# Kernel optimization log

Hardware: AMD Instinct MI355X
Metric: run time of the kernel (lower is better)

The kernel has to match this reference:

```python
import jax, jax.numpy as jnp
import numpy as np

B, S, DE, DR, H, V, R, L = 16, 128, 192, 64, 256, 100000, 64, 12
CAP = 20            # max tree depth enforced at generation time
NLEV = CAP + 1      # number of bottom-up levels (heights 0..CAP)


def setup_inputs() -> dict:
    rng = np.random.default_rng(0)
    # random dependency trees: node 0 is root, parent(i) in [0, i)
    heads = np.full((B, S), -1, np.int64)
    depth = np.zeros((B, S), np.int64)
    for b in range(B):
        for i in range(1, S):
            p = int(rng.integers(0, i))
            if depth[b, p] >= CAP:
                p = 0
            heads[b, i] = p
            depth[b, i] = depth[b, p] + 1
    # height = distance from deepest descendant leaf (leaves: 0)
    height = np.zeros((B, S), np.int64)
    for b in range(B):
        for i in range(S - 1, 0, -1):
            p = heads[b, i]
            if height[b, p] < height[b, i] + 1:
                height[b, p] = height[b, i] + 1
    base = (np.arange(B) * S)[:, None]
    child_idx = (base + np.arange(1, S)[None, :]).reshape(-1)   # [B*(S-1)]
    parent_idx = (base + heads[:, 1:]).reshape(-1)              # [B*(S-1)]

    key = jax.random.key(0)
    ks = jax.random.split(key, 16)
    u = lambda k, shape: jax.random.uniform(k, shape, jnp.float32, -0.08, 0.08)
    DIN = DE + DR
    return {
        "xs": jax.random.randint(ks[0], (B, S), 0, V),
        "rels": jax.random.randint(ks[1], (B, S), 0, R),
        "child_idx": jnp.asarray(child_idx),
        "parent_idx": jnp.asarray(parent_idx),
        "node_height": jnp.asarray(height.reshape(-1)),
        "n_levels": NLEV,
        "emb_W": u(ks[2], (V, DE)),
        "rel_W": u(ks[3], (R, DR)),
        "W_ix": u(ks[4], (DIN, H)), "b_ix": jnp.zeros((H,), jnp.float32),
        "W_ih": u(ks[5], (H, H)),   "b_ih": jnp.zeros((H,), jnp.float32),
        "W_fx": u(ks[6], (DIN, H)), "b_fx": jnp.zeros((H,), jnp.float32),
        "W_fh": u(ks[7], (H, H)),   "b_fh": jnp.zeros((H,), jnp.float32),
        "W_ox": u(ks[8], (DIN, H)), "W_oh": u(ks[9], (H, H)),
        "W_ux": u(ks[10], (DIN, H)), "W_uh": u(ks[11], (H, H)),
        "W_out": u(ks[12], (H, L)), "b_out": jnp.zeros((L,), jnp.float32),
    }


def reference(xs, rels, child_idx, parent_idx, node_height, n_levels,
              emb_W, rel_W, W_ix, b_ix, W_ih, b_ih, W_fx, b_fx, W_fh, b_fh,
              W_ox, W_oh, W_ux, W_uh, W_out, b_out):
    Bs, Ss = xs.shape
    N = Bs * Ss
    Hh = W_ih.shape[0]
    # embed + concat (dropout = identity in eval mode), flatten trees
    x = jnp.concatenate([emb_W[xs], rel_W[rels]], axis=-1).reshape(N, -1)  # [N, DIN]
    # input-side projections are level-invariant: hoist out of the recurrence
    ix = x @ W_ix + b_ix
    fx = x @ W_fx + b_fx
    ox = x @ W_ox
    ux = x @ W_ux

    h0 = jnp.zeros((N, Hh), x.dtype)
    c0 = jnp.zeros((N, Hh), x.dtype)

    def step(carry, level):
        h, c = carry
        h_ch = h[child_idx]                                   # [E, H]
        c_ch = c[child_idx]
        h_sum = jax.ops.segment_sum(h_ch, parent_idx, num_segments=N)
        # per-child forget gate (ChildSum); zero-padded children of the
        # original contribute f*0 = 0, so edges-only is exact
        f_e = jax.nn.sigmoid(h_ch @ W_fh + b_fh + fx[parent_idx])
        fc = jax.ops.segment_sum(f_e * c_ch, parent_idx, num_segments=N)
        i = jax.nn.sigmoid(ix + h_sum @ W_ih + b_ih)
        o = jax.nn.sigmoid(ox + h_sum @ W_oh)
        u_ = jnp.tanh(ux + h_sum @ W_uh)
        c_new = i * u_ + fc
        h_new = o * jnp.tanh(c_new)
        m = (node_height == level)[:, None]                   # commit this level only
        return (jnp.where(m, h_new, h), jnp.where(m, c_new, c)), None

    (h, _), _ = jax.lax.scan(step, (h0, c0), jnp.arange(n_levels))
    pooled = jnp.max(h.reshape(Bs, Ss, Hh), axis=1)           # max_pool1d over time
    return pooled @ W_out + b_out
```

## Files before the change

kernel.cpp:

```cpp
#include <hip/hip_runtime.h>
#include <hip/hip_bf16.h>

#define NN   2048
#define BB   16
#define SS   128
#define HH   256
#define DE   192
#define DR   64
#define DIN  256
#define LOUT 12
#define NLEV 21
#define TE   127

#define NT   16
#define CB   16
#define WC   16
#define RB   16
#define EB   32
#define CPAD 260
#define KP   264

#define SENT64 0xFFFFFFFFFFFFFFFFULL

typedef unsigned long long ull;
typedef __attribute__((ext_vector_type(8))) short short8v;
typedef __attribute__((ext_vector_type(4))) float f32x4;

__device__ __forceinline__ float sigm(float x){ return 1.f/(1.f + __expf(-x)); }

__device__ __forceinline__ short f2bf(float f){
    union { __hip_bfloat16 b; short s; } v; v.b = __float2bfloat16(f); return v.s;
}
__device__ __forceinline__ float bf2f(short s){
    union { unsigned u; float f; } v; v.u = ((unsigned)(unsigned short)s) << 16; return v.f;
}
__device__ __forceinline__ void st_dev(ull* p, ull v){
    __hip_atomic_store(p, v, __ATOMIC_RELAXED, __HIP_MEMORY_SCOPE_AGENT);
}
__device__ __forceinline__ ull ld_dev(const ull* p){
    return __hip_atomic_load(p, __ATOMIC_RELAXED, __HIP_MEMORY_SCOPE_AGENT);
}
__device__ __forceinline__ void st_devf(float* p, float v){
    __hip_atomic_store(p, v, __ATOMIC_RELAXED, __HIP_MEMORY_SCOPE_AGENT);
}
__device__ __forceinline__ int ld_devi(const int* p){
    return __hip_atomic_load(p, __ATOMIC_RELAXED, __HIP_MEMORY_SCOPE_AGENT);
}

__device__ __forceinline__ void barrier_lds(){
    __builtin_amdgcn_sched_barrier(0);
    asm volatile("s_waitcnt lgkmcnt(0)" ::: "memory");
    __builtin_amdgcn_s_barrier();
    __builtin_amdgcn_sched_barrier(0);
}

template<int N>
__device__ __forceinline__ void stageN(const ull* __restrict__ src,
                                       ull* __restrict__ dst){
    ull u[N];
    #pragma unroll
    for (int q = 0; q < N; ++q) u[q] = ld_dev(&src[q]);
    for (;;) {
        bool bad = false;
        #pragma unroll
        for (int q = 0; q < N; ++q) bad = bad || (u[q] == SENT64);
        if (!bad) break;
        __builtin_amdgcn_s_sleep(1);
        #pragma unroll
        for (int q = 0; q < N; ++q)
            if (u[q] == SENT64) u[q] = ld_dev(&src[q]);
    }
    #pragma unroll
    for (int q = 0; q < N; ++q) dst[q] = u[q];
}

__device__ __forceinline__ f32x4 mm16(const short* __restrict__ A,
                                      const short* __restrict__ B, int lane){
    f32x4 acc = {0.f, 0.f, 0.f, 0.f};
    const int ro = (lane & 15) * KP + ((lane >> 4) << 3);
    #pragma unroll
    for (int k0 = 0; k0 < 256; k0 += 32)
        acc = __builtin_amdgcn_mfma_f32_16x16x32_bf16(
            *(const short8v*)(A + ro + k0),
            *(const short8v*)(B + ro + k0),
            acc, 0, 0, 0);
    return acc;
}

__device__ __forceinline__ void publish4(float hv, int cc, ull* rowp, int col0){
    unsigned p = (unsigned short)f2bf(hv);
    unsigned q = (unsigned)__shfl_xor((int)p, 1);
    unsigned pr = p | (q << 16);
    unsigned pr2 = (unsigned)__shfl_xor((int)pr, 2);
    if ((cc & 3) == 0)
        st_dev(rowp + ((col0 + cc) >> 2), pr | ((ull)pr2 << 32));
}

__global__ __launch_bounds__(256) void fill_k(ull* __restrict__ hx,
                                              int* __restrict__ pb)
{
    const int t = threadIdx.x;
    const size_t base = (size_t)blockIdx.x * 512 + t;
    st_dev(&hx[base], SENT64);
    st_dev(&hx[base + 256], SENT64);
    if (blockIdx.x == 0) {
        #pragma unroll
        for (int q = 0; q < (BB*HH)/256; ++q)
            __hip_atomic_store(&pb[q*256 + t], -1, __ATOMIC_RELAXED,
                               __HIP_MEMORY_SCOPE_AGENT);
    }
}

__global__ __launch_bounds__(256, 1) void tree_k(
    const int* __restrict__ xs, const int* __restrict__ rels,
    const float* __restrict__ emb_W, const float* __restrict__ rel_W,
    const float* __restrict__ W_ix, const float* __restrict__ b_ix,
    const float* __restrict__ W_fx, const float* __restrict__ b_fx,
    const float* __restrict__ W_ox, const float* __restrict__ W_ux,
    const int* __restrict__ child_idx, const int* __restrict__ parent_idx,
    const int* __restrict__ node_height,
    const float* __restrict__ W_ih, const float* __restrict__ b_ih,
    const float* __restrict__ W_fh, const float* __restrict__ b_fh,
    const float* __restrict__ W_oh, const float* __restrict__ W_uh,
    ull* __restrict__ hx, float* __restrict__ poolbuf,
    const float* __restrict__ W_out, const float* __restrict__ b_out,
    float* __restrict__ out)
{
    __shared__ short Wbf[4*WC*KP];
    __shared__ float projL[4][SS][WC];
    __shared__ float cloc[SS][WC+1];
    __shared__ float hloc[SS][WC+1];
    __shared__ float biasF[WC], biasI[WC];
    __shared__ int loff[SS+1], lcur[SS], llist[SS];
    __shared__ int lvoff[NLEV+1], lvcur[NLEV], lvnodes[SS];
    __shared__ int chs[EB], slts[EB], csum[RB+1], nodes_s[RB];
    __shared__ int s_maxH;
    extern __shared__ __align__(16) char trans[];
    short* xbf       = (short*)trans;
    short* hstage_bf = (short*)trans;
    float* hsN       = (float*)(trans + EB*KP*2);
    short* hsN_bf    = (short*)(trans + EB*KP*2 + RB*CPAD*4);
    float* part      = (float*)(trans + EB*KP*2 + RB*CPAD*4 + RB*KP*2);
    float* fcN       = part + 3*RB*17;

    const int t    = threadIdx.x;
    const int bid  = blockIdx.x;
    const int xcd  = bid & 7;
    const int idx  = bid >> 3;
    const int b    = xcd + 8 * (idx >> 4);
    const int cgp  = idx & 15;
    const int col0 = cgp * WC;
    const int cc   = t & 15;
    const int rr   = t >> 4;
    const int wv   = t >> 6;
    const int lane = t & 63;

    if (t < SS) { llist[t] = xs[b*SS + t]; lvnodes[t] = rels[b*SS + t]; lcur[t] = 0; }
    if (t < NLEV) lvcur[t] = 0;
    if (t == 0)   s_maxH = 0;
    __syncthreads();

    for (int r = wv*32; r < wv*32 + 32; ++r) {
        float4 v;
        if (lane < 48) v = *(const float4*)&emb_W[(long long)llist[r]*DE + lane*4];
        else           v = *(const float4*)&rel_W[(long long)lvnodes[r]*DR + (lane-48)*4];
        union { short s[4]; ull u; } pk;
        pk.s[0] = f2bf(v.x); pk.s[1] = f2bf(v.y);
        pk.s[2] = f2bf(v.z); pk.s[3] = f2bf(v.w);
        *(ull*)&xbf[r*KP + lane*4] = pk.u;
    }
    {
        const float* Wm4[4] = { W_fh, W_ih, W_oh, W_uh };
        for (int m = 0; m < 4; ++m) {
            short* dst = Wbf + (m*WC + cc)*KP;
            const float* src = Wm4[m] + col0 + cc;
            #pragma unroll 4
            for (int kb = 0; kb < 16; ++kb) {
                int k = kb*16 + rr;
                dst[k] = f2bf(src[(long long)k*HH]);
            }
        }
        if (t < WC) { biasF[t] = b_fh[col0+t]; biasI[t] = b_ih[col0+t]; }
    }
    __syncthreads();

    if (t < TE) { int p = parent_idx[b*TE + t] - b*SS; atomicAdd(&lcur[p], 1); }
    if (t < SS) { int hg = node_height[b*SS + t]; atomicAdd(&lvcur[hg], 1); atomicMax(&s_maxH, hg); }
    {
        const float* Wxm = (wv==0) ? W_ix : (wv==1) ? W_fx : (wv==2) ? W_ox : W_ux;
        const int ccl = lane & 15, kg = lane >> 4;
        short8v bfr[8];
        #pragma unroll
        for (int f = 0; f < 8; ++f) {
            #pragma unroll
            for (int j = 0; j < 8; ++j)
                bfr[f][j] = f2bf(Wxm[(long long)(f*32 + kg*8 + j)*HH + col0 + ccl]);
        }
        const float bias = (wv==0) ? b_ix[col0+ccl] : (wv==1) ? b_fx[col0+ccl] : 0.f;
        for (int ch = 0; ch < 8; ++ch) {
            f32x4 acc = {0.f,0.f,0.f,0.f};
            const short* ap = xbf + (ch*16 + ccl)*KP + kg*8;
            #pragma unroll
            for (int f = 0; f < 8; ++f)
                acc = __builtin_amdgcn_mfma_f32_16x16x32_bf16(
                    *(const short8v*)(ap + f*32), bfr[f], acc, 0,0,0);
            #pragma unroll
            for (int r = 0; r < 4; ++r)
                projL[wv][ch*16 + kg*4 + r][ccl] = acc[r] + bias;
        }
    }
    __syncthreads();

    if (t == 0) {
        int off = 0;
        for (int i = 0; i < SS; ++i) { int v = lcur[i]; loff[i] = off; lcur[i] = off; off += v; }
        loff[SS] = off;
        off = 0;
        for (int l2 = 0; l2 < NLEV; ++l2) { int v = lvcur[l2]; lvoff[l2] = off; lvcur[l2] = off; off += v; }
        lvoff[NLEV] = off;
    }
    __syncthreads();
    if (t < TE) {
        int e = b*TE + t;
        int p = parent_idx[e] - b*SS;
        int pos = atomicAdd(&lcur[p], 1);
        llist[pos] = child_idx[e] - b*SS;
    }
    if (t < SS) {
        int hg = node_height[b*SS + t];
        int pos = atomicAdd(&lvcur[hg], 1);
        lvnodes[pos] = t;
    }
    __syncthreads();

    const int mH = s_maxH;
    for (int lev = 0; lev <= mH; ++lev) {
        const int s0 = lvoff[lev], s1 = lvoff[lev+1];
        int fastE = -1;
        if (lev > 0 && s1 - s0 == 1) {
            int n0 = lvnodes[s0];
            fastE = loff[n0+1] - loff[n0];
        }

        if (lev == 0) {
            for (int cs = s0; cs < s1; cs += RB) {
                int nbN = min(RB, s1 - cs);
                if (rr < nbN) {
                    int n = lvnodes[cs + rr];
                    float iv = sigm(projL[0][n][cc] + biasI[cc]);
                    float ov = sigm(projL[2][n][cc]);
                    float uv = tanhf(projL[3][n][cc]);
                    float cv = iv * uv;
                    float hv = ov * tanhf(cv);
                    cloc[n][cc] = cv; hloc[n][cc] = hv;
                    publish4(hv, cc, hx + (size_t)(b*SS + n)*64, col0);
                }
            }
        }
        else if (fastE > 0 && fastE <= RB) {
            const int n = lvnodes[s0];
            const int off = loff[n];
            const int E = fastE;
            if (t < E)  chs[t] = llist[off + t];
            if (t < WC) fcN[t] = 0.f;
            barrier_lds();
            if (rr < E)
                stageN<4>(hx + (size_t)(b*SS + chs[rr])*64 + cc*4,
                          (ull*)(hstage_bf + rr*KP + cc*16));
            barrier_lds();
            {
                const int ccl = lane & 15, kg = lane >> 4, rbase = kg << 2;
                if (wv == 0) {
                    f32x4 acc = mm16(hstage_bf, Wbf, lane);
                    #pragma unroll
                    for (int r = 0; r < 4; ++r) {
                        int e = rbase + r;
                        if (e < E) {
                            float f = sigm(acc[r] + biasF[ccl] + projL[1][n][ccl]);
                            atomicAdd(&fcN[ccl], f * cloc[chs[e]][ccl]);
                        }
                    }
                } else {
                    f32x4 acc = {0.f,0.f,0.f,0.f};
                    const short* wm = Wbf + (wv*WC + ccl)*KP + kg*8;
                    for (int f = 0; f < 8; ++f) {
                        float s[8] = {0,0,0,0,0,0,0,0};
                        for (int e = 0; e < E; ++e) {
                            short8v xv = *(const short8v*)(hstage_bf + e*KP + f*32 + kg*8);
                            #pragma unroll
                            for (int j = 0; j < 8; ++j) s[j] += bf2f(xv[j]);
                        }
                        short8v af;
                        #pragma unroll
                        for (int j = 0; j < 8; ++j) af[j] = f2bf(s[j]);
                        acc = __builtin_amdgcn_mfma_f32_16x16x32_bf16(
                            af, *(const short8v*)(wm + f*32), acc, 0,0,0);
                    }
                    if (kg == 0) part[((wv-1)*RB)*17 + ccl] = acc[0];
                }
            }
            barrier_lds();
            if (t < WC) {
                float iv = sigm(projL[0][n][t] + part[0*17 + t] + biasI[t]);
                float ov = sigm(projL[2][n][t] + part[(1*RB)*17 + t]);
                float uv = tanhf(projL[3][n][t] + part[(2*RB)*17 + t]);
                float cv = iv*uv + fcN[t];
                float hv = ov * tanhf(cv);
                cloc[n][t] = cv; hloc[n][t] = hv;
                publish4(hv, t, hx + (size_t)(b*SS + n)*64, col0);
            }
        }
        else {
            for (int cs = s0; cs < s1; cs += RB) {
                const int nbN = min(RB, s1 - cs);
                if (t < nbN) {
                    int n = lvnodes[cs + t];
                    nodes_s[t] = n;
                    csum[t+1] = loff[n+1] - loff[n];
                }
                if (t == 0) csum[0] = 0;
                barrier_lds();
                if (t == 0) for (int i = 1; i <= nbN; ++i) csum[i] += csum[i-1];
                for (int r2 = 0; r2 < nbN; ++r2) hsN[r2*CPAD + t] = 0.f;
                fcN[rr*17 + cc] = 0.f;
                barrier_lds();

                const int Ech = csum[nbN];
                for (int eb = 0; eb < Ech; eb += EB) {
                    const int m = min(EB, Ech - eb);
                    if (t < m) {
                        int e = eb + t;
                        int s2 = 0;
                        while (csum[s2+1] <= e) ++s2;
                        chs[t]  = llist[loff[nodes_s[s2]] + (e - csum[s2])];
                        slts[t] = s2;
                    }
                    barrier_lds();
                    if (m <= 16) {
                        if (rr < m)
                            stageN<4>(hx + (size_t)(b*SS + chs[rr])*64 + cc*4,
                                      (ull*)(hstage_bf + rr*KP + cc*16));
                    } else {
                        int row = t >> 3, q = t & 7;
                        if (row < m)
                            stageN<8>(hx + (size_t)(b*SS + chs[row])*64 + q*8,
                                      (ull*)(hstage_bf + row*KP + q*32));
                    }
                    barrier_lds();
                    const bool lastc = (eb + EB >= Ech);
                    if (wv < 2) {
                        if (wv*16 < m) {
                            const int ccl = lane & 15, rbase = (lane >> 4) << 2;
                            f32x4 acc = mm16(hstage_bf + wv*16*KP, Wbf, lane);
                            #pragma unroll
                            for (int r = 0; r < 4; ++r) {
                                int e = wv*16 + rbase + r;
                                if (e < m) {
                                    int sl = slts[e];
                                    float f = sigm(acc[r] + biasF[ccl]
                                                   + projL[1][nodes_s[sl]][ccl]);
                                    atomicAdd(&fcN[sl*17 + ccl],
                                              f * cloc[chs[e]][ccl]);
                                }
                            }
                        }
                    } else {
                        const int kk = (t - 128) * 2;
                        float a0 = 0.f, a1 = 0.f;
                        int cur = slts[0];
                        for (int jj = 0; jj < m; ++jj) {
                            int s2 = slts[jj];
                            if (s2 != cur) {
                                hsN[cur*CPAD + kk]     += a0;
                                hsN[cur*CPAD + kk + 1] += a1;
                                a0 = a1 = 0.f; cur = s2;
                            }
                            unsigned v = *(const unsigned*)&hstage_bf[jj*KP + kk];
                            a0 += bf2f((short)(v & 0xFFFF));
                            a1 += bf2f((short)(v >> 16));
                        }
                        hsN[cur*CPAD + kk]     += a0;
                        hsN[cur*CPAD + kk + 1] += a1;
                        if (lastc) {
                            for (int s2 = 0; s2 < nbN; ++s2) {
                                hsN_bf[s2*KP + kk]     = f2bf(hsN[s2*CPAD + kk]);
                                hsN_bf[s2*KP + kk + 1] = f2bf(hsN[s2*CPAD + kk + 1]);
                            }
                        }
                    }
                    barrier_lds();
                }

                if (wv >= 1) {
                    const int ccl = lane & 15, rbase = (lane >> 4) << 2;
                    f32x4 acc = mm16(hsN_bf, Wbf + (wv*WC)*KP, lane);
                    #pragma unroll
                    for (int r = 0; r < 4; ++r)
                        part[((wv-1)*RB + rbase + r)*17 + ccl] = acc[r];
                }
                barrier_lds();
                if (rr < nbN) {
                    int n = nodes_s[rr];
                    float iv = sigm(projL[0][n][cc] + part[(0*RB + rr)*17 + cc] + biasI[cc]);
                    float ov = sigm(projL[2][n][cc] + part[(1*RB + rr)*17 + cc]);
                    float uv = tanhf(projL[3][n][cc] + part[(2*RB + rr)*17 + cc]);
                    float cv = iv*uv + fcN[rr*17 + cc];
                    float hv = ov * tanhf(cv);
                    cloc[n][cc] = cv; hloc[n][cc] = hv;
                    publish4(hv, cc, hx + (size_t)(b*SS + n)*64, col0);
                }
                barrier_lds();
            }
        }
        barrier_lds();
    }

    {
        float mx = -3.4e38f;
        for (int s2 = rr; s2 < SS; s2 += RB)
            mx = fmaxf(mx, hloc[s2][cc]);
        part[rr*17 + cc] = mx;
        __syncthreads();
        if (t < WC) {
            float m2 = part[0*17 + t];
            #pragma unroll
            for (int r2 = 1; r2 < RB; ++r2) m2 = fmaxf(m2, part[r2*17 + t]);
            st_devf(&poolbuf[b*HH + col0 + t], m2);
        }
    }
    if (cgp == 0) {
        const int* pb = (const int*)poolbuf + b*HH + t;
        int w = ld_devi(pb);
        while (w == -1) { __builtin_amdgcn_s_sleep(1); w = ld_devi(pb); }
        float* pl = (float*)trans;
        pl[t] = __int_as_float(w);
        __syncthreads();
        if (t < LOUT) {
            float acc = b_out[t];
            for (int k = 0; k < HH; ++k)
                acc += pl[k] * W_out[k*LOUT + t];
            out[b*LOUT + t] = acc;
        }
    }
}

extern "C" void kernel_launch(void* const* d_in, const int* in_sizes, int n_in,
                              void* d_out, int out_size, void* d_ws, size_t ws_size,
                              hipStream_t stream)
{
    const int* xs          = (const int*)d_in[0];
    const int* rels        = (const int*)d_in[1];
    const int* child_idx   = (const int*)d_in[2];
    const int* parent_idx  = (const int*)d_in[3];
    const int* node_height = (const int*)d_in[4];
    const float* emb_W = (const float*)d_in[6];
    const float* rel_W = (const float*)d_in[7];
    const float* W_ix  = (const float*)d_in[8];
    const float* b_ix  = (const float*)d_in[9];
    const float* W_ih  = (const float*)d_in[10];
    const float* b_ih  = (const float*)d_in[11];
    const float* W_fx  = (const float*)d_in[12];
    const float* b_fx  = (const float*)d_in[13];
    const float* W_fh  = (const float*)d_in[14];
    const float* b_fh  = (const float*)d_in[15];
    const float* W_ox  = (const float*)d_in[16];
    const float* W_oh  = (const float*)d_in[17];
    const float* W_ux  = (const float*)d_in[18];
    const float* W_uh  = (const float*)d_in[19];
    const float* W_out = (const float*)d_in[20];
    const float* b_out = (const float*)d_in[21];

    ull*   hx      = (ull*)d_ws;
    float* poolbuf = (float*)((char*)d_ws + (size_t)NN*64*8);

    fill_k<<<256, 256, 0, stream>>>(hx, (int*)poolbuf);

    const unsigned int shmem = (unsigned int)(SS * KP * 2);
    tree_k<<<dim3(NT*CB), dim3(256), shmem, stream>>>(
        xs, rels, emb_W, rel_W,
        W_ix, b_ix, W_fx, b_fx, W_ox, W_ux,
        child_idx, parent_idx, node_height,
        W_ih, b_ih, W_fh, b_fh, W_oh, W_uh,
        hx, poolbuf,
        W_out, b_out, (float*)d_out);
}
```

Measured before the change: 235.2 us.

## Process each tree node per wavefront with register-resident weight fragments and no block barriers

Restructures the per-level recurrence so each of the four wavefronts handles one node independently. Each wave gathers that node's children into its own LDS stage, computes forget gates and the child-sum with MFMA against weight fragments held in registers, and prefetches the next node's children while finishing the current one. This removes the block-wide barriers, atomics and child-slot bookkeeping inside each level, and the input projection is split into two halves to shrink the LDS footprint. In exchange it uses many more registers, and levels with fewer than four nodes leave waves idle.

```diff
diff --git a/kernel.cpp b/kernel.cpp
--- a/kernel.cpp
+++ b/kernel.cpp
@@ -16,8 +16,6 @@
 #define CB   16
 #define WC   16
 #define RB   16
-#define EB   32
-#define CPAD 260
 #define KP   264
 
 #define SENT64 0xFFFFFFFFFFFFFFFFULL
@@ -52,39 +50,6 @@
     asm volatile("s_waitcnt lgkmcnt(0)" ::: "memory");
     __builtin_amdgcn_s_barrier();
     __builtin_amdgcn_sched_barrier(0);
-}
-
-template<int N>
-__device__ __forceinline__ void stageN(const ull* __restrict__ src,
-                                       ull* __restrict__ dst){
-    ull u[N];
-    #pragma unroll
-    for (int q = 0; q < N; ++q) u[q] = ld_dev(&src[q]);
-    for (;;) {
-        bool bad = false;
-        #pragma unroll
-        for (int q = 0; q < N; ++q) bad = bad || (u[q] == SENT64);
-        if (!bad) break;
-        __builtin_amdgcn_s_sleep(1);
-        #pragma unroll
-        for (int q = 0; q < N; ++q)
-            if (u[q] == SENT64) u[q] = ld_dev(&src[q]);
-    }
-    #pragma unroll
-    for (int q = 0; q < N; ++q) dst[q] = u[q];
-}
-
-__device__ __forceinline__ f32x4 mm16(const short* __restrict__ A,
-                                      const short* __restrict__ B, int lane){
-    f32x4 acc = {0.f, 0.f, 0.f, 0.f};
-    const int ro = (lane & 15) * KP + ((lane >> 4) << 3);
-    #pragma unroll
-    for (int k0 = 0; k0 < 256; k0 += 32)
-        acc = __builtin_amdgcn_mfma_f32_16x16x32_bf16(
-            *(const short8v*)(A + ro + k0),
-            *(const short8v*)(B + ro + k0),
-            acc, 0, 0, 0);
-    return acc;
 }
 
 __device__ __forceinline__ void publish4(float hv, int cc, ull* rowp, int col0){
@@ -126,22 +91,18 @@
     const float* __restrict__ W_out, const float* __restrict__ b_out,
     float* __restrict__ out)
 {
-    __shared__ short Wbf[4*WC*KP];
+    extern __shared__ __align__(16) char trans[];
+    short* Wbf    = (short*)trans;
+    short* hstage = (short*)(trans + 4*WC*KP*2);
+
     __shared__ float projL[4][SS][WC];
     __shared__ float cloc[SS][WC+1];
     __shared__ float hloc[SS][WC+1];
+    __shared__ short hsrow[4][KP];
     __shared__ float biasF[WC], biasI[WC];
     __shared__ int loff[SS+1], lcur[SS], llist[SS];
     __shared__ int lvoff[NLEV+1], lvcur[NLEV], lvnodes[SS];
-    __shared__ int chs[EB], slts[EB], csum[RB+1], nodes_s[RB];
     __shared__ int s_maxH;
-    extern __shared__ __align__(16) char trans[];
-    short* xbf       = (short*)trans;
-    short* hstage_bf = (short*)trans;
-    float* hsN       = (float*)(trans + EB*KP*2);
-    short* hsN_bf    = (short*)(trans + EB*KP*2 + RB*CPAD*4);
-    float* part      = (float*)(trans + EB*KP*2 + RB*CPAD*4 + RB*KP*2);
-    float* fcN       = part + 3*RB*17;
 
     const int t    = threadIdx.x;
     const int bid  = blockIdx.x;
@@ -154,21 +115,16 @@
     const int rr   = t >> 4;
     const int wv   = t >> 6;
     const int lane = t & 63;
+    const int col  = lane & 15;
+    const int kg   = lane >> 4;
 
     if (t < SS) { llist[t] = xs[b*SS + t]; lvnodes[t] = rels[b*SS + t]; lcur[t] = 0; }
     if (t < NLEV) lvcur[t] = 0;
     if (t == 0)   s_maxH = 0;
     __syncthreads();
 
-    for (int r = wv*32; r < wv*32 + 32; ++r) {
-        float4 v;
-        if (lane < 48) v = *(const float4*)&emb_W[(long long)llist[r]*DE + lane*4];
-        else           v = *(const float4*)&rel_W[(long long)lvnodes[r]*DR + (lane-48)*4];
-        union { short s[4]; ull u; } pk;
-        pk.s[0] = f2bf(v.x); pk.s[1] = f2bf(v.y);
-        pk.s[2] = f2bf(v.z); pk.s[3] = f2bf(v.w);
-        *(ull*)&xbf[r*KP + lane*4] = pk.u;
-    }
+    if (t < TE) { int p = parent_idx[b*TE + t] - b*SS; atomicAdd(&lcur[p], 1); }
+    if (t < SS) { int hg = node_height[b*SS + t]; atomicAdd(&lvcur[hg], 1); atomicMax(&s_maxH, hg); }
     {
         const float* Wm4[4] = { W_fh, W_ih, W_oh, W_uh };
         for (int m = 0; m < 4; ++m) {
@@ -182,34 +138,56 @@
         }
         if (t < WC) { biasF[t] = b_fh[col0+t]; biasI[t] = b_ih[col0+t]; }
     }
-    __syncthreads();
-
-    if (t < TE) { int p = parent_idx[b*TE + t] - b*SS; atomicAdd(&lcur[p], 1); }
-    if (t < SS) { int hg = node_height[b*SS + t]; atomicAdd(&lvcur[hg], 1); atomicMax(&s_maxH, hg); }
+    short8v bfr[8];
     {
         const float* Wxm = (wv==0) ? W_ix : (wv==1) ? W_fx : (wv==2) ? W_ox : W_ux;
-        const int ccl = lane & 15, kg = lane >> 4;
-        short8v bfr[8];
         #pragma unroll
         for (int f = 0; f < 8; ++f) {
             #pragma unroll
             for (int j = 0; j < 8; ++j)
-                bfr[f][j] = f2bf(Wxm[(long long)(f*32 + kg*8 + j)*HH + col0 + ccl]);
-        }
-        const float bias = (wv==0) ? b_ix[col0+ccl] : (wv==1) ? b_fx[col0+ccl] : 0.f;
-        for (int ch = 0; ch < 8; ++ch) {
+                bfr[f][j] = f2bf(Wxm[(long long)(f*32 + kg*8 + j)*HH + col0 + col]);
+        }
+    }
+    const float pbias = (wv==0) ? b_ix[col0+col] : (wv==1) ? b_fx[col0+col] : 0.f;
+
+    short* xbf = hstage;
+    for (int half = 0; half < 2; ++half) {
+        __syncthreads();
+        #pragma unroll
+        for (int r2 = 0; r2 < 16; ++r2) {
+            int gr = half*64 + wv*16 + r2;
+            float4 v;
+            if (lane < 48) v = *(const float4*)&emb_W[(long long)llist[gr]*DE + lane*4];
+            else           v = *(const float4*)&rel_W[(long long)lvnodes[gr]*DR + (lane-48)*4];
+            union { short s[4]; ull u; } pk;
+            pk.s[0] = f2bf(v.x); pk.s[1] = f2bf(v.y);
+            pk.s[2] = f2bf(v.z); pk.s[3] = f2bf(v.w);
+            *(ull*)&xbf[(wv*16 + r2)*KP + lane*4] = pk.u;
+        }
+        __syncthreads();
+        for (int lch = 0; lch < 4; ++lch) {
             f32x4 acc = {0.f,0.f,0.f,0.f};
-            const short* ap = xbf + (ch*16 + ccl)*KP + kg*8;
+            const short* ap = xbf + (lch*16 + col)*KP + kg*8;
             #pragma unroll
             for (int f = 0; f < 8; ++f)
                 acc = __builtin_amdgcn_mfma_f32_16x16x32_bf16(
                     *(const short8v*)(ap + f*32), bfr[f], acc, 0,0,0);
             #pragma unroll
             for (int r = 0; r < 4; ++r)
-                projL[wv][ch*16 + kg*4 + r][ccl] = acc[r] + bias;
+                projL[wv][half*64 + lch*16 + kg*4 + r][col] = acc[r] + pbias;
         }
     }
     __syncthreads();
+
+    short8v wfrF[8], wfrI[8], wfrO[8], wfrU[8];
+    #pragma unroll
+    for (int f = 0; f < 8; ++f) {
+        const int o = col*KP + f*32 + kg*8;
+        wfrF[f] = *(const short8v*)(Wbf + (0*WC)*KP + o);
+        wfrI[f] = *(const short8v*)(Wbf + (1*WC)*KP + o);
+        wfrO[f] = *(const short8v*)(Wbf + (2*WC)*KP + o);
+        wfrU[f] = *(const short8v*)(Wbf + (3*WC)*KP + o);
+    }
 
     if (t == 0) {
         int off = 0;
@@ -233,198 +211,172 @@
     }
     __syncthreads();
 
+    short* Hst = hstage + wv*16*KP;
     const int mH = s_maxH;
     for (int lev = 0; lev <= mH; ++lev) {
         const int s0 = lvoff[lev], s1 = lvoff[lev+1];
-        int fastE = -1;
-        if (lev > 0 && s1 - s0 == 1) {
-            int n0 = lvnodes[s0];
-            fastE = loff[n0+1] - loff[n0];
-        }
 
         if (lev == 0) {
-            for (int cs = s0; cs < s1; cs += RB) {
-                int nbN = min(RB, s1 - cs);
-                if (rr < nbN) {
-                    int n = lvnodes[cs + rr];
-                    float iv = sigm(projL[0][n][cc] + biasI[cc]);
-                    float ov = sigm(projL[2][n][cc]);
-                    float uv = tanhf(projL[3][n][cc]);
+            for (int it = 0; s0 + it*16 + wv*4 < s1; ++it) {
+                int j2 = s0 + it*16 + wv*4 + kg;
+                if (j2 < s1) {
+                    int n = lvnodes[j2];
+                    float iv = sigm(projL[0][n][col] + biasI[col]);
+                    float ov = sigm(projL[2][n][col]);
+                    float uv = tanhf(projL[3][n][col]);
                     float cv = iv * uv;
                     float hv = ov * tanhf(cv);
-                    cloc[n][cc] = cv; hloc[n][cc] = hv;
-                    publish4(hv, cc, hx + (size_t)(b*SS + n)*64, col0);
+                    cloc[n][col] = cv; hloc[n][col] = hv;
+                    publish4(hv, col, hx + (size_t)(b*SS + n)*64, col0);
                 }
             }
-        }
-        else if (fastE > 0 && fastE <= RB) {
-            const int n = lvnodes[s0];
-            const int off = loff[n];
-            const int E = fastE;
-            if (t < E)  chs[t] = llist[off + t];
-            if (t < WC) fcN[t] = 0.f;
-            barrier_lds();
-            if (rr < E)
-                stageN<4>(hx + (size_t)(b*SS + chs[rr])*64 + cc*4,
-                          (ull*)(hstage_bf + rr*KP + cc*16));
-            barrier_lds();
-            {
-                const int ccl = lane & 15, kg = lane >> 4, rbase = kg << 2;
-                if (wv == 0) {
-                    f32x4 acc = mm16(hstage_bf, Wbf, lane);
+        } else {
+            int j = s0 + wv;
+            ull u[16]; int chr[4];
+            int nOff = 0, nE = 0;
+            if (j < s1) {
+                int n0 = lvnodes[j]; nOff = loff[n0]; nE = loff[n0+1] - nOff;
+                int m0 = min(nE, 16);
+                #pragma unroll
+                for (int rw = 0; rw < 4; ++rw) {
+                    int e = kg + rw*4;
+                    chr[rw] = (e < m0) ? llist[nOff + e] : -1;
+                    if (chr[rw] >= 0) {
+                        const ull* sp = hx + (size_t)(b*SS + chr[rw])*64 + col*4;
+                        #pragma unroll
+                        for (int q = 0; q < 4; ++q) u[rw*4+q] = ld_dev(sp+q);
+                    }
+                }
+            }
+            while (j < s1) {
+                const int n = lvnodes[j];
+                const int off = nOff, E = nE;
+                float hs0=0.f, hs1=0.f, hs2=0.f, hs3=0.f, fpart=0.f;
+                for (int fr = 0; fr < E; fr += 16) {
+                    const int m = min(16, E - fr);
+                    if (fr > 0) {
+                        #pragma unroll
+                        for (int rw = 0; rw < 4; ++rw) {
+                            int e = kg + rw*4;
+                            chr[rw] = (e < m) ? llist[off + fr + e] : -1;
+                            if (chr[rw] >= 0) {
+                                const ull* sp = hx + (size_t)(b*SS + chr[rw])*64 + col*4;
+                                #pragma unroll
+                                for (int q = 0; q < 4; ++q) u[rw*4+q] = ld_dev(sp+q);
+                            }
+                        }
+                    }
+                    for (;;) {
+                        bool bad = false;
+                        #pragma unroll
+                        for (int rw = 0; rw < 4; ++rw)
+                            if (chr[rw] >= 0) {
+                                #pragma unroll
+                                for (int q = 0; q < 4; ++q)
+                                    bad = bad || (u[rw*4+q] == SENT64);
+                            }
+                        if (!bad) break;
+                        __builtin_amdgcn_s_sleep(1);
+                        #pragma unroll
+                        for (int rw = 0; rw < 4; ++rw)
+                            if (chr[rw] >= 0) {
+                                const ull* sp = hx + (size_t)(b*SS + chr[rw])*64 + col*4;
+                                #pragma unroll
+                                for (int q = 0; q < 4; ++q)
+                                    if (u[rw*4+q] == SENT64) u[rw*4+q] = ld_dev(sp+q);
+                            }
+                    }
+                    #pragma unroll
+                    for (int rw = 0; rw < 4; ++rw)
+                        if (chr[rw] >= 0) {
+                            int e = kg + rw*4;
+                            ull* dp = (ull*)&Hst[e*KP + col*16];
+                            dp[0]=u[rw*4]; dp[1]=u[rw*4+1]; dp[2]=u[rw*4+2]; dp[3]=u[rw*4+3];
+                        }
+                    f32x4 fa = {0.f,0.f,0.f,0.f};
+                    {
+                        const int ro = col*KP + kg*8;
+                        #pragma unroll
+                        for (int f = 0; f < 8; ++f)
+                            fa = __builtin_amdgcn_mfma_f32_16x16x32_bf16(
+                                *(const short8v*)(Hst + ro + f*32), wfrF[f], fa, 0,0,0);
+                    }
                     #pragma unroll
                     for (int r = 0; r < 4; ++r) {
-                        int e = rbase + r;
-                        if (e < E) {
-                            float f = sigm(acc[r] + biasF[ccl] + projL[1][n][ccl]);
-                            atomicAdd(&fcN[ccl], f * cloc[chs[e]][ccl]);
+                        int e = kg*4 + r;
+                        if (e < m) {
+                            int ch2 = llist[off + fr + e];
+                            float fg = sigm(fa[r] + biasF[col] + projL[1][n][col]);
+                            fpart += fg * cloc[ch2][col];
                         }
                     }
-                } else {
-                    f32x4 acc = {0.f,0.f,0.f,0.f};
-                    const short* wm = Wbf + (wv*WC + ccl)*KP + kg*8;
+                    for (int e = 0; e < m; ++e) {
+                        union { short s[4]; ull v; } rv;
+                        rv.v = *(const ull*)&Hst[e*KP + lane*4];
+                        hs0 += bf2f(rv.s[0]); hs1 += bf2f(rv.s[1]);
+                        hs2 += bf2f(rv.s[2]); hs3 += bf2f(rv.s[3]);
+                    }
+                }
+                int jn = j + 4;
+                if (jn < s1) {
+                    int n1 = lvnodes[jn]; nOff = loff[n1]; nE = loff[n1+1] - nOff;
+                    int m1 = min(nE, 16);
+                    #pragma unroll
+                    for (int rw = 0; rw < 4; ++rw) {
+                        int e = kg + rw*4;
+                        chr[rw] = (e < m1) ? llist[nOff + e] : -1;
+                        if (chr[rw] >= 0) {
+                            const ull* sp = hx + (size_t)(b*SS + chr[rw])*64 + col*4;
+                            #pragma unroll
+                            for (int q = 0; q < 4; ++q) u[rw*4+q] = ld_dev(sp+q);
+                        }
+                    }
+                }
+                {
+                    union { short s[4]; ull v; } hp;
+                    hp.s[0]=f2bf(hs0); hp.s[1]=f2bf(hs1);
+                    hp.s[2]=f2bf(hs2); hp.s[3]=f2bf(hs3);
+                    *(ull*)&hsrow[wv][lane*4] = hp.v;
+                }
+                f32x4 ia={0.f,0.f,0.f,0.f}, oa={0.f,0.f,0.f,0.f}, ua={0.f,0.f,0.f,0.f};
+                {
+                    const short* H = &hsrow[wv][0];
+                    #pragma unroll
                     for (int f = 0; f < 8; ++f) {
-                        float s[8] = {0,0,0,0,0,0,0,0};
-                        for (int e = 0; e < E; ++e) {
-                            short8v xv = *(const short8v*)(hstage_bf + e*KP + f*32 + kg*8);
-                            #pragma unroll
-                            for (int j = 0; j < 8; ++j) s[j] += bf2f(xv[j]);
-                        }
-                        short8v af;
-                        #pragma unroll
-                        for (int j = 0; j < 8; ++j) af[j] = f2bf(s[j]);
-                        acc = __builtin_amdgcn_mfma_f32_16x16x32_bf16(
-                            af, *(const short8v*)(wm + f*32), acc, 0,0,0);
-                    }
-                    if (kg == 0) part[((wv-1)*RB)*17 + ccl] = acc[0];
-                }
+                        short8v af = *(const short8v*)(H + f*32 + kg*8);
+                        ia = __builtin_amdgcn_mfma_f32_16x16x32_bf16(af, wfrI[f], ia, 0,0,0);
+                        oa = __builtin_amdgcn_mfma_f32_16x16x32_bf16(af, wfrO[f], oa, 0,0,0);
+                        ua = __builtin_amdgcn_mfma_f32_16x16x32_bf16(af, wfrU[f], ua, 0,0,0);
+                    }
+                }
+                fpart += __shfl_xor(fpart, 16);
+                fpart += __shfl_xor(fpart, 32);
+                if (lane < 16) {
+                    float iv = sigm(projL[0][n][lane] + ia[0] + biasI[lane]);
+                    float ov = sigm(projL[2][n][lane] + oa[0]);
+                    float uv = tanhf(projL[3][n][lane] + ua[0]);
+                    float cv = iv*uv + fpart;
+                    float hv = ov * tanhf(cv);
+                    cloc[n][lane] = cv; hloc[n][lane] = hv;
+                    publish4(hv, lane, hx + (size_t)(b*SS + n)*64, col0);
+                }
+                j = jn;
             }
-            barrier_lds();
-            if (t < WC) {
-                float iv = sigm(projL[0][n][t] + part[0*17 + t] + biasI[t]);
-                float ov = sigm(projL[2][n][t] + part[(1*RB)*17 + t]);
-                float uv = tanhf(projL[3][n][t] + part[(2*RB)*17 + t]);
-                float cv = iv*uv + fcN[t];
-                float hv = ov * tanhf(cv);
-                cloc[n][t] = cv; hloc[n][t] = hv;
-                publish4(hv, t, hx + (size_t)(b*SS + n)*64, col0);
-            }
-        }
-        else {
-            for (int cs = s0; cs < s1; cs += RB) {
-                const int nbN = min(RB, s1 - cs);
-                if (t < nbN) {
-                    int n = lvnodes[cs + t];
-                    nodes_s[t] = n;
-                    csum[t+1] = loff[n+1] - loff[n];
-                }
-                if (t == 0) csum[0] = 0;
-                barrier_lds();
-                if (t == 0) for (int i = 1; i <= nbN; ++i) csum[i] += csum[i-1];
-                for (int r2 = 0; r2 < nbN; ++r2) hsN[r2*CPAD + t] = 0.f;
-                fcN[rr*17 + cc] = 0.f;
-                barrier_lds();
-
-                const int Ech = csum[nbN];
-                for (int eb = 0; eb < Ech; eb += EB) {
-                    const int m = min(EB, Ech - eb);
-                    if (t < m) {
-                        int e = eb + t;
-                        int s2 = 0;
-                        while (csum[s2+1] <= e) ++s2;
-                        chs[t]  = llist[loff[nodes_s[s2]] + (e - csum[s2])];
-                        slts[t] = s2;
-                    }
-                    barrier_lds();
-                    if (m <= 16) {
-                        if (rr < m)
-                            stageN<4>(hx + (size_t)(b*SS + chs[rr])*64 + cc*4,
-                                      (ull*)(hstage_bf + rr*KP + cc*16));
-                    } else {
-                        int row = t >> 3, q = t & 7;
-                        if (row < m)
-                            stageN<8>(hx + (size_t)(b*SS + chs[row])*64 + q*8,
-                                      (ull*)(hstage_bf + row*KP + q*32));
-                    }
-                    barrier_lds();
-                    const bool lastc = (eb + EB >= Ech);
-                    if (wv < 2) {
-                        if (wv*16 < m) {
-                            const int ccl = lane & 15, rbase = (lane >> 4) << 2;
-                            f32x4 acc = mm16(hstage_bf + wv*16*KP, Wbf, lane);
-                            #pragma unroll
-                            for (int r = 0; r < 4; ++r) {
-                                int e = wv*16 + rbase + r;
-                                if (e < m) {
-                                    int sl = slts[e];
-                                    float f = sigm(acc[r] + biasF[ccl]
-                                                   + projL[1][nodes_s[sl]][ccl]);
-                                    atomicAdd(&fcN[sl*17 + ccl],
-                                              f * cloc[chs[e]][ccl]);
-                                }
-                            }
-                        }
-                    } else {
-                        const int kk = (t - 128) * 2;
-                        float a0 = 0.f, a1 = 0.f;
-                        int cur = slts[0];
-                        for (int jj = 0; jj < m; ++jj) {
-                            int s2 = slts[jj];
-                            if (s2 != cur) {
-                                hsN[cur*CPAD + kk]     += a0;
-                                hsN[cur*CPAD + kk + 1] += a1;
-                                a0 = a1 = 0.f; cur = s2;
-                            }
-                            unsigned v = *(const unsigned*)&hstage_bf[jj*KP + kk];
-                            a0 += bf2f((short)(v & 0xFFFF));
-                            a1 += bf2f((short)(v >> 16));
-                        }
-                        hsN[cur*CPAD + kk]     += a0;
-                        hsN[cur*CPAD + kk + 1] += a1;
-                        if (lastc) {
-                            for (int s2 = 0; s2 < nbN; ++s2) {
-                                hsN_bf[s2*KP + kk]     = f2bf(hsN[s2*CPAD + kk]);
-                                hsN_bf[s2*KP + kk + 1] = f2bf(hsN[s2*CPAD + kk + 1]);
-                            }
-                        }
-                    }
-                    barrier_lds();
-                }
-
-                if (wv >= 1) {
-                    const int ccl = lane & 15, rbase = (lane >> 4) << 2;
-                    f32x4 acc = mm16(hsN_bf, Wbf + (wv*WC)*KP, lane);
-                    #pragma unroll
-                    for (int r = 0; r < 4; ++r)
-                        part[((wv-1)*RB + rbase + r)*17 + ccl] = acc[r];
-                }
-                barrier_lds();
-                if (rr < nbN) {
-                    int n = nodes_s[rr];
-                    float iv = sigm(projL[0][n][cc] + part[(0*RB + rr)*17 + cc] + biasI[cc]);
-                    float ov = sigm(projL[2][n][cc] + part[(1*RB + rr)*17 + cc]);
-                    float uv = tanhf(projL[3][n][cc] + part[(2*RB + rr)*17 + cc]);
-                    float cv = iv*uv + fcN[rr*17 + cc];
-                    float hv = ov * tanhf(cv);
-                    cloc[n][cc] = cv; hloc[n][cc] = hv;
-                    publish4(hv, cc, hx + (size_t)(b*SS + n)*64, col0);
-                }
-                barrier_lds();
-            }
         }
         barrier_lds();
     }
 
     {
+        float* pp = (float*)hstage;
         float mx = -3.4e38f;
         for (int s2 = rr; s2 < SS; s2 += RB)
             mx = fmaxf(mx, hloc[s2][cc]);
-        part[rr*17 + cc] = mx;
+        pp[rr*17 + cc] = mx;
         __syncthreads();
         if (t < WC) {
-            float m2 = part[0*17 + t];
+            float m2 = pp[0*17 + t];
             #pragma unroll
-            for (int r2 = 1; r2 < RB; ++r2) m2 = fmaxf(m2, part[r2*17 + t]);
+            for (int r2 = 1; r2 < RB; ++r2) m2 = fmaxf(m2, pp[r2*17 + t]);
             st_devf(&poolbuf[b*HH + col0 + t], m2);
         }
     }
@@ -432,7 +384,7 @@
         const int* pb = (const int*)poolbuf + b*HH + t;
         int w = ld_devi(pb);
         while (w == -1) { __builtin_amdgcn_s_sleep(1); w = ld_devi(pb); }
-        float* pl = (float*)trans;
+        float* pl = (float*)&hsrow[0][0];
         pl[t] = __int_as_float(w);
         __syncthreads();
         if (t < LOUT) {
@@ -475,7 +427,7 @@
 
     fill_k<<<256, 256, 0, stream>>>(hx, (int*)poolbuf);
 
-    const unsigned int shmem = (unsigned int)(SS * KP * 2);
+    const unsigned int shmem = (unsigned int)(8u * WC * KP * 2);
     tree_k<<<dim3(NT*CB), dim3(256), shmem, stream>>>(
         xs, rels, emb_W, rel_W,
         W_ix, b_ix, W_fx, b_fx, W_ox, W_ux,
```

Result: faster. 229.7 us (-2.3%).
